# Performance work log

Measured on AMD Instinct MI355X. Metric: run time of the kernel, lower is better.

## Reference

```python
import jax, jax.numpy as jnp
import numpy as np

B, SQ, SK, D = 8, 2048, 2048, 128


def setup_inputs() -> dict:
    key = jax.random.key(0)
    kq, kk, kv = jax.random.split(key, 3)
    Q = jax.random.normal(kq, (B, SQ, D), dtype=jnp.float32)
    K = jax.random.normal(kk, (B, SK, D), dtype=jnp.float32)
    V = jax.random.normal(kv, (B, SK, D), dtype=jnp.float32)
    return {"Q": Q, "K": K, "V": V}


def reference(Q, K, V):
    d_k = K.shape[2]  # NOTE: module divides by d_k, not sqrt(d_k)
    # scores: [B, Sq, Sk]
    scores = jnp.einsum('bqd,bkd->bqk', Q, K) / d_k
    # unconventional softmax over the batch dim (dim=0), as in the source
    attn = jax.nn.softmax(scores, axis=0)
    # output: [B, Sq, D]
    return jnp.einsum('bqk,bkd->bqd', attn, V)
```

## Files before the change

### kernel.cpp

```cpp
#include <hip/hip_runtime.h>
#include <hip/hip_bf16.h>

#define B_   8
#define SQ_  2048
#define SK_  2048
#define D_   128

typedef __attribute__((ext_vector_type(8))) _Float16 f16x8;
typedef __attribute__((ext_vector_type(4))) _Float16 f16x4;
typedef __attribute__((ext_vector_type(4))) float    f32x4;

#define QK_BSTRIDE (128 * 4 * 64 * 8)
#define VF_BSTRIDE (64 * 8 * 64 * 8)

__device__ __forceinline__ void dma16(const void* g, void* l) {
    __builtin_amdgcn_global_load_lds(
        (const __attribute__((address_space(1))) unsigned int*)g,
        (__attribute__((address_space(3))) unsigned int*)l, 16, 0, 0);
}

__device__ __forceinline__ float fast_exp2(float x) {
#if __has_builtin(__builtin_amdgcn_exp2f)
    return __builtin_amdgcn_exp2f(x);
#else
    return __expf(x * 0.6931471805599453f);
#endif
}

__global__ __launch_bounds__(256)
void prep(const float* __restrict__ Q, const float* __restrict__ K,
          const float* __restrict__ V,
          _Float16* __restrict__ Qf, _Float16* __restrict__ Kf,
          _Float16* __restrict__ Vf) {
    __shared__ _Float16 T[64][136];
    const int bid = blockIdx.x;
    if (bid < 2048) {
        const float* src = (bid >= 1024) ? K : Q;
        _Float16*    dst = (bid >= 1024) ? Kf : Qf;
        const float sc = (bid >= 1024) ? 0.0625f : 0.18033688f;
        int gid = (bid & 1023) * 256 + threadIdx.x;
        int l  = gid & 63;
        int ks = (gid >> 6) & 3;
        int t  = (gid >> 8) & 127;
        int b  = gid >> 15;
        const float* p = src + ((size_t)b * 2048 + t * 16 + (l & 15)) * 128
                             + ks * 32 + (l >> 4) * 8;
        f32x4 a = *(const f32x4*)p;
        f32x4 c = *(const f32x4*)(p + 4);
        f16x8 r;
        r[0] = (_Float16)(a[0] * sc); r[1] = (_Float16)(a[1] * sc);
        r[2] = (_Float16)(a[2] * sc); r[3] = (_Float16)(a[3] * sc);
        r[4] = (_Float16)(c[0] * sc); r[5] = (_Float16)(c[1] * sc);
        r[6] = (_Float16)(c[2] * sc); r[7] = (_Float16)(c[3] * sc);
        *(f16x8*)(dst + (size_t)gid * 8) = r;
    } else {
        const int vb = bid - 2048;
        const int b  = vb >> 5;
        const int kb = vb & 31;
        const int t  = threadIdx.x;
        const int row = t >> 2, c0 = (t & 3) * 32;
        const float* src = V + ((size_t)b * SK_ + kb * 64 + row) * D_ + c0;
#pragma unroll
        for (int u = 0; u < 8; ++u) {
            f32x4 v = *(const f32x4*)(src + u * 4);
            f16x4 h;
            h[0] = (_Float16)v[0]; h[1] = (_Float16)v[1];
            h[2] = (_Float16)v[2]; h[3] = (_Float16)v[3];
            *(f16x4*)&T[row][c0 + u * 4] = h;
        }
        __syncthreads();
#pragma unroll
        for (int u = 0; u < 4; ++u) {
            int s   = u * 256 + t;
            int l   = s & 63;
            int dt  = (s >> 6) & 7;
            int ktl = s >> 9;
            int hi  = l >> 4, ql = l & 15;
            f16x8 r;
#pragma unroll
            for (int j = 0; j < 8; ++j) r[j] = T[ktl * 32 + hi * 8 + j][dt * 16 + ql];
            *(f16x8*)(Vf + (((size_t)b * 64 + kb * 2 + ktl) * 8 + dt) * 512 + (size_t)l * 8) = r;
        }
    }
}

__global__ __launch_bounds__(512, 4)
void zred(const _Float16* __restrict__ Qf, const _Float16* __restrict__ Kf,
          _Float16* __restrict__ Pf, int nqt, int qoff16) {
    __shared__ __attribute__((aligned(16))) _Float16 E[8][64][64];
    const int bid   = blockIdx.x;
    const int qtile = bid >> 5;
    const int ktile = bid & 31;
    const int b  = threadIdx.x >> 6;
    const int l  = threadIdx.x & 63;
    const int hi = l >> 4, ql = l & 15;

    const _Float16* Qb = Qf + (size_t)b * QK_BSTRIDE;
    const _Float16* Kb = Kf + (size_t)b * QK_BSTRIDE;

    f32x4 s[4][4] = {};
    __builtin_amdgcn_s_setprio(1);
#pragma unroll
    for (int ks = 0; ks < 4; ++ks) {
        f16x8 kf[4];
#pragma unroll
        for (int kk = 0; kk < 4; ++kk)
            kf[kk] = *(const f16x8*)(Kb + ((((size_t)ktile * 4 + kk) * 4 + ks) * 64 + l) * 8);
#pragma unroll
        for (int qq = 0; qq < 4; ++qq) {
            f16x8 qv = *(const f16x8*)(Qb + ((((size_t)(qoff16 + qtile * 4 + qq)) * 4 + ks) * 64 + l) * 8);
#pragma unroll
            for (int kk = 0; kk < 4; ++kk)
                s[kk][qq] = __builtin_amdgcn_mfma_f32_16x16x32_f16(kf[kk], qv, s[kk][qq], 0, 0, 0);
        }
    }
    __builtin_amdgcn_s_setprio(0);

    f16x4* E4 = (f16x4*)&E[0][0][0];
#pragma unroll
    for (int kk = 0; kk < 4; ++kk)
#pragma unroll
        for (int qq = 0; qq < 4; ++qq) {
            f16x4 e;
#pragma unroll
            for (int r = 0; r < 4; ++r)
                e[r] = (_Float16)fast_exp2(s[kk][qq][r]);
            int q = qq * 16 + ql;
            int k = kk * 16 + hi * 4;
            int g16 = ((b * 64 + q) << 3) + ((k >> 3) ^ (q & 7));
            E4[g16 * 2 + ((k >> 2) & 1)] = e;
        }
    __syncthreads();

    const int t    = threadIdx.x;
    const int ktl  = t >> 8;
    const int qq2  = (t >> 6) & 3;
    const int l2   = t & 63;
    const int hi2  = l2 >> 4, ql2 = l2 & 15;
    const int q_loc  = qq2 * 16 + ql2;
    const int k0_loc = ktl * 32 + hi2 * 8;
    const f16x8* E8  = (const f16x8*)&E[0][0][0];
    const int eidx   = (q_loc << 3) + ((k0_loc >> 3) ^ (q_loc & 7));

    f16x8 z = E8[eidx];
#pragma unroll
    for (int bb = 1; bb < 8; ++bb) z = z + E8[bb * 512 + eidx];
    float inv[8];
#pragma unroll
    for (int j = 0; j < 8; ++j) inv[j] = __builtin_amdgcn_rcpf((float)z[j]);

    const size_t pbase = (((size_t)(qtile * 4 + qq2)) * 64 + (ktile * 2 + ktl)) * 512 + (size_t)l2 * 8;
#pragma unroll
    for (int bb = 0; bb < 8; ++bb) {
        f16x8 e = E8[bb * 512 + eidx];
        f16x8 p;
#pragma unroll
        for (int j = 0; j < 8; ++j) p[j] = (_Float16)((float)e[j] * inv[j]);
        *(f16x8*)(Pf + (size_t)bb * nqt * 32768 + pbase) = p;
    }
}

__global__ __launch_bounds__(512)
void av(const _Float16* __restrict__ Pf, const _Float16* __restrict__ Vf,
        float* __restrict__ out, int nqt, int qoff) {
    __shared__ __attribute__((aligned(16))) _Float16 lds[3 * 12288];

    const int bid = blockIdx.x;
    const int b   = bid & 7;
    const int mt  = bid >> 3;
    const int w   = threadIdx.x >> 6;
    const int l   = threadIdx.x & 63;
    const int wq  = w >> 2;
    const int wd  = w & 3;
    const int hi  = l >> 4, ql = l & 15;

    const _Float16* Pb = Pf + (size_t)b * nqt * 32768;
    const _Float16* Vb = Vf + (size_t)b * VF_BSTRIDE;

#define STAGE(bufi, kt2) do {                                                  \
    _Float16* dst0 = (_Float16*)lds + (size_t)(bufi) * 12288;                  \
    _Pragma("unroll")                                                          \
    for (int u = 0; u < 3; ++u) {                                              \
        int c = w * 3 + u;                                                     \
        const _Float16* srcp;                                                  \
        if (c < 8)                                                             \
            srcp = Pb + (((size_t)(mt * 4 + (c >> 1))) * 64 + ((kt2) * 2 + (c & 1))) * 512 + (size_t)l * 8; \
        else {                                                                 \
            int cv = c - 8;                                                    \
            srcp = Vb + (((size_t)((kt2) * 2 + (cv >> 3))) * 8 + (cv & 7)) * 512 + (size_t)l * 8; \
        }                                                                      \
        dma16(srcp, dst0 + c * 512);                                           \
    }                                                                          \
} while (0)

#define MFMA_PHASE(bufi) do {                                                  \
    const _Float16* Bf = (const _Float16*)lds + (size_t)(bufi) * 12288;        \
    _Pragma("unroll")                                                          \
    for (int ktl = 0; ktl < 2; ++ktl) {                                        \
        f16x8 pfr[2], vfr[2];                                                  \
        _Pragma("unroll")                                                      \
        for (int i = 0; i < 2; ++i)                                            \
            pfr[i] = *(const f16x8*)(Bf + ((wq * 2 + i) * 2 + ktl) * 512 + l * 8); \
        _Pragma("unroll")                                                      \
        for (int j = 0; j < 2; ++j)                                            \
            vfr[j] = *(const f16x8*)(Bf + 4096 + (ktl * 8 + wd * 2 + j) * 512 + l * 8); \
        _Pragma("unroll")                                                      \
        for (int i = 0; i < 2; ++i)                                            \
            _Pragma("unroll")                                                  \
            for (int j = 0; j < 2; ++j)                                        \
                acc[i][j] = __builtin_amdgcn_mfma_f32_16x16x32_f16(pfr[i], vfr[j], acc[i][j], 0, 0, 0); \
    }                                                                          \
} while (0)

    f32x4 acc[2][2] = {};
    STAGE(0, 0);
    STAGE(1, 1);
    for (int kt2 = 0; kt2 < 32; ++kt2) {
        if (kt2 < 30) {
            STAGE((kt2 + 2) % 3, kt2 + 2);
            asm volatile("s_waitcnt vmcnt(6)" ::: "memory");
        } else if (kt2 == 30) {
            asm volatile("s_waitcnt vmcnt(3)" ::: "memory");
        } else {
            asm volatile("s_waitcnt vmcnt(0)" ::: "memory");
        }
        __builtin_amdgcn_s_barrier();
        __builtin_amdgcn_sched_barrier(0);
        __builtin_amdgcn_s_setprio(1);
        MFMA_PHASE(kt2 % 3);
        __builtin_amdgcn_s_setprio(0);
        __builtin_amdgcn_s_barrier();
    }

    const int q0 = qoff + mt * 64 + wq * 32;
#pragma unroll
    for (int i = 0; i < 2; ++i)
#pragma unroll
        for (int j = 0; j < 2; ++j)
#pragma unroll
            for (int r = 0; r < 4; ++r)
                out[((size_t)b * SQ_ + q0 + i * 16 + hi * 4 + r) * D_ + (wd * 2 + j) * 16 + ql]
                    = acc[i][j][r];
#undef STAGE
#undef MFMA_PHASE
}

extern "C" void kernel_launch(void* const* d_in, const int* in_sizes, int n_in,
                              void* d_out, int out_size, void* d_ws, size_t ws_size,
                              hipStream_t stream) {
    const float* Q = (const float*)d_in[0];
    const float* K = (const float*)d_in[1];
    const float* V = (const float*)d_in[2];
    float* out = (float*)d_out;

    _Float16* Qf = (_Float16*)d_ws;
    _Float16* Kf = Qf + (size_t)B_ * QK_BSTRIDE;
    _Float16* Vf = Kf + (size_t)B_ * QK_BSTRIDE;
    _Float16* Pf = Vf + (size_t)B_ * VF_BSTRIDE;

    size_t used  = (size_t)(12 * 1024 * 1024);
    size_t avail = ws_size > used ? (ws_size - used) / 2 : 0;
    int nq = 2048;
    while (nq > 64 && (size_t)nq * 16384 > avail) nq >>= 1;
    int nchunks = 2048 / nq;
    int nqt = nq / 16;

    prep<<<2048 + 256, 256, 0, stream>>>(Q, K, V, Qf, Kf, Vf);

    for (int ci = 0; ci < nchunks; ++ci) {
        int qoff = ci * nq;
        zred<<<(nq / 64) * 32, 512, 0, stream>>>(Qf, Kf, Pf, nqt, qoff >> 4);
        av<<<(nq / 64) * 8, 512, 0, stream>>>(Pf, Vf, out, nqt, qoff);
    }
}
```

Measured before the change: 59.11 us.

## Deepen AV pipeline to four LDS buffers and transpose Q/K prep via LDS

```diff
diff --git a/kernel.cpp b/kernel.cpp
--- a/kernel.cpp
+++ b/kernel.cpp
@@ -34,30 +34,39 @@
           _Float16* __restrict__ Vf) {
     __shared__ _Float16 T[64][136];
     const int bid = blockIdx.x;
-    if (bid < 2048) {
-        const float* src = (bid >= 1024) ? K : Q;
-        _Float16*    dst = (bid >= 1024) ? Kf : Qf;
-        const float sc = (bid >= 1024) ? 0.0625f : 0.18033688f;
-        int gid = (bid & 1023) * 256 + threadIdx.x;
-        int l  = gid & 63;
-        int ks = (gid >> 6) & 3;
-        int t  = (gid >> 8) & 127;
-        int b  = gid >> 15;
-        const float* p = src + ((size_t)b * 2048 + t * 16 + (l & 15)) * 128
-                             + ks * 32 + (l >> 4) * 8;
-        f32x4 a = *(const f32x4*)p;
-        f32x4 c = *(const f32x4*)(p + 4);
-        f16x8 r;
-        r[0] = (_Float16)(a[0] * sc); r[1] = (_Float16)(a[1] * sc);
-        r[2] = (_Float16)(a[2] * sc); r[3] = (_Float16)(a[3] * sc);
-        r[4] = (_Float16)(c[0] * sc); r[5] = (_Float16)(c[1] * sc);
-        r[6] = (_Float16)(c[2] * sc); r[7] = (_Float16)(c[3] * sc);
-        *(f16x8*)(dst + (size_t)gid * 8) = r;
+    const int t   = threadIdx.x;
+    if (bid < 512) {
+        const int tens = bid >> 8;
+        const float* src = tens ? K : Q;
+        _Float16*    dst = tens ? Kf : Qf;
+        const float  sc  = tens ? 0.0625f : 0.18033688f;
+        const int b  = (bid >> 5) & 7;
+        const int rb = bid & 31;
+        const int row = t >> 2, c0 = (t & 3) * 32;
+        const float* srow = src + ((size_t)b * 2048 + rb * 64 + row) * 128 + c0;
+#pragma unroll
+        for (int u = 0; u < 32; u += 4) {
+            f32x4 v = *(const f32x4*)(srow + u);
+            f16x4 h;
+            h[0] = (_Float16)(v[0] * sc); h[1] = (_Float16)(v[1] * sc);
+            h[2] = (_Float16)(v[2] * sc); h[3] = (_Float16)(v[3] * sc);
+            *(f16x4*)&T[row][c0 + u] = h;
+        }
+        __syncthreads();
+#pragma unroll
+        for (int u = 0; u < 4; ++u) {
+            int c  = u * 256 + t;
+            int l  = c & 63;
+            int ks = (c >> 6) & 3;
+            int qt = c >> 8;
+            int hi = l >> 4, ql = l & 15;
+            f16x8 r = *(const f16x8*)&T[qt * 16 + ql][ks * 32 + hi * 8];
+            *(f16x8*)(dst + ((((size_t)b * 128 + rb * 4 + qt) * 4 + ks) * 64 + l) * 8) = r;
+        }
     } else {
-        const int vb = bid - 2048;
+        const int vb = bid - 512;
         const int b  = vb >> 5;
         const int kb = vb & 31;
-        const int t  = threadIdx.x;
         const int row = t >> 2, c0 = (t & 3) * 32;
         const float* src = V + ((size_t)b * SK_ + kb * 64 + row) * D_ + c0;
 #pragma unroll
@@ -163,7 +172,7 @@
 __global__ __launch_bounds__(512)
 void av(const _Float16* __restrict__ Pf, const _Float16* __restrict__ Vf,
         float* __restrict__ out, int nqt, int qoff) {
-    __shared__ __attribute__((aligned(16))) _Float16 lds[3 * 12288];
+    __shared__ __attribute__((aligned(16))) _Float16 lds[4 * 12288];
 
     const int bid = blockIdx.x;
     const int b   = bid & 7;
@@ -215,21 +224,17 @@
     f32x4 acc[2][2] = {};
     STAGE(0, 0);
     STAGE(1, 1);
+    STAGE(2, 2);
     for (int kt2 = 0; kt2 < 32; ++kt2) {
-        if (kt2 < 30) {
-            STAGE((kt2 + 2) % 3, kt2 + 2);
-            asm volatile("s_waitcnt vmcnt(6)" ::: "memory");
-        } else if (kt2 == 30) {
-            asm volatile("s_waitcnt vmcnt(3)" ::: "memory");
-        } else {
-            asm volatile("s_waitcnt vmcnt(0)" ::: "memory");
-        }
+        if (kt2 <= 29)      asm volatile("s_waitcnt vmcnt(6)" ::: "memory");
+        else if (kt2 == 30) asm volatile("s_waitcnt vmcnt(3)" ::: "memory");
+        else                asm volatile("s_waitcnt vmcnt(0)" ::: "memory");
         __builtin_amdgcn_s_barrier();
         __builtin_amdgcn_sched_barrier(0);
+        if (kt2 < 29) STAGE((kt2 + 3) & 3, kt2 + 3);
         __builtin_amdgcn_s_setprio(1);
-        MFMA_PHASE(kt2 % 3);
+        MFMA_PHASE(kt2 & 3);
         __builtin_amdgcn_s_setprio(0);
-        __builtin_amdgcn_s_barrier();
     }
 
     const int q0 = qoff + mt * 64 + wq * 32;
@@ -265,7 +270,7 @@
     int nchunks = 2048 / nq;
     int nqt = nq / 16;
 
-    prep<<<2048 + 256, 256, 0, stream>>>(Q, K, V, Qf, Kf, Vf);
+    prep<<<768, 256, 0, stream>>>(Q, K, V, Qf, Kf, Vf);
 
     for (int ci = 0; ci < nchunks; ++ci) {
         int qoff = ci * nq;
```

Measured after the change: 57.45 us. -2.8%, faster.
